# Optimization experiments

Hardware: AMD Instinct MI355X
Metric: run time of the kernel (lower is better)

Reference implementation:

```python
import jax, jax.numpy as jnp
import numpy as np

D_MODEL = 1024
NUM_HEADS = 16
OMEGA_0 = 30.0
D_K = D_MODEL // NUM_HEADS


def _siren_uniform(key, shape, fan_in, omega_0=OMEGA_0):
    bound = np.sqrt(6.0 / fan_in) / omega_0
    return jax.random.uniform(key, shape, minval=-bound, maxval=bound, dtype=jnp.float32)


def setup_inputs() -> dict:
    key = jax.random.key(0)
    ks = jax.random.split(key, 9)
    B, S = 2, 2048
    x = jax.random.normal(ks[0], (B, S, D_MODEL), dtype=jnp.float32)
    # weights stored as (out, in) like torch nn.Linear
    Wq = _siren_uniform(ks[1], (D_MODEL, D_MODEL), D_MODEL)
    bq = _siren_uniform(ks[2], (D_MODEL,), D_MODEL)
    Wk = _siren_uniform(ks[3], (D_MODEL, D_MODEL), D_MODEL)
    bk = _siren_uniform(ks[4], (D_MODEL,), D_MODEL)
    Wv = _siren_uniform(ks[5], (D_MODEL, D_MODEL), D_MODEL)
    bv = _siren_uniform(ks[6], (D_MODEL,), D_MODEL)
    Wo = _siren_uniform(ks[7], (D_MODEL, D_MODEL), D_MODEL)
    bo = _siren_uniform(ks[8], (D_MODEL,), D_MODEL)
    return {"x": x, "Wq": Wq, "bq": bq, "Wk": Wk, "bk": bk,
            "Wv": Wv, "bv": bv, "Wo": Wo, "bo": bo}


def reference(x, Wq, bq, Wk, bk, Wv, bv, Wo, bo):
    B, S, _ = x.shape
    scale = np.sqrt(D_K).astype(np.float32)
    # project and split heads: (B, H, S, d_k)
    def proj(W, b):
        y = jnp.einsum('bsd,ed->bse', x, W) + b
        return y.reshape(B, S, NUM_HEADS, D_K).transpose(0, 2, 1, 3)
    Q = proj(Wq, bq)
    K = proj(Wk, bk)
    V = proj(Wv, bv)
    logits = jnp.einsum('bhqd,bhkd->bhqk', Q, K) / scale
    attn = jnp.sin(OMEGA_0 * logits)  # no normalization
    out = jnp.einsum('bhqk,bhkd->bhqd', attn, V)
    out = out.transpose(0, 2, 1, 3).reshape(B, S, D_MODEL)
    return jnp.einsum('bsd,ed->bse', out, Wo) + bo
```

## Files before the change

### kernel.cpp

```cpp
#include <hip/hip_runtime.h>
#include <stdint.h>

typedef __attribute__((ext_vector_type(8))) __bf16 fragAB;
typedef __attribute__((ext_vector_type(4))) float f32x4;

__device__ __forceinline__ unsigned short f2bf(float f) {
    union { float f; unsigned int u; } v; v.f = f;
    unsigned int u = v.u + 0x7fffu + ((v.u >> 16) & 1u);
    return (unsigned short)(u >> 16);
}

__device__ __forceinline__ f32x4 MFMA(fragAB a, fragAB b, f32x4 c) {
    return __builtin_amdgcn_mfma_f32_16x16x32_bf16(a, b, c, 0, 0, 0);
}

__device__ __forceinline__ void gl16(const void* g, void* l) {
    __builtin_amdgcn_global_load_lds((const __attribute__((address_space(1))) void*)g,
                                     (__attribute__((address_space(3))) void*)l, 16, 0, 0);
}

__device__ __forceinline__ float fsin_rev(float rev) {
    float r; asm("v_sin_f32 %0, %1" : "=v"(r) : "v"(rev)); return r;
}
__device__ __forceinline__ unsigned int cvtpk(float lo, float hi) {
    unsigned int r; asm("v_cvt_pk_bf16_f32 %0, %1, %2" : "=v"(r) : "v"(lo), "v"(hi)); return r;
}

__global__ __launch_bounds__(256) void cvt_all(
    const float* __restrict__ x,  const float* __restrict__ wq, const float* __restrict__ wk,
    const float* __restrict__ wv, const float* __restrict__ wo,
    unsigned short* __restrict__ xb,  unsigned short* __restrict__ wqb, unsigned short* __restrict__ wkb,
    unsigned short* __restrict__ wvb, unsigned short* __restrict__ wob)
{
    const int bid = blockIdx.x;
    const float* s; unsigned short* d; int off;
    if (bid < 4096)      { s = x;  d = xb;  off = bid; }
    else if (bid < 5120) { s = wq; d = wqb; off = bid - 4096; }
    else if (bid < 6144) { s = wk; d = wkb; off = bid - 5120; }
    else if (bid < 7168) { s = wv; d = wvb; off = bid - 6144; }
    else                 { s = wo; d = wob; off = bid - 7168; }
    const int i = (off * 256 + threadIdx.x) * 4;
    float4 f = *(const float4*)(s + i);
    ushort4 o;
    o.x = f2bf(f.x); o.y = f2bf(f.y); o.z = f2bf(f.z); o.w = f2bf(f.w);
    *(ushort4*)(d + i) = o;
}

__global__ __launch_bounds__(256, 2)
void gemm_k(const unsigned short* __restrict__ A,
            const unsigned short* __restrict__ W0, const unsigned short* __restrict__ W1,
            const unsigned short* __restrict__ W2,
            const float* __restrict__ b0, const float* __restrict__ b1, const float* __restrict__ b2,
            void* o0, void* o1, void* o2, int md0, int md1, int md2)
{
    __shared__ unsigned short As[8192];
    __shared__ unsigned short Ws[8192];

    const int z = blockIdx.z;
    const unsigned short* W = z == 0 ? W0 : (z == 1 ? W1 : W2);
    const float* bias        = z == 0 ? b0 : (z == 1 ? b1 : b2);
    void* out                = z == 0 ? o0 : (z == 1 ? o1 : o2);
    const int mode           = z == 0 ? md0 : (z == 1 ? md1 : md2);

    const int t = threadIdx.x;
    const int lane = t & 63;
    const int g = lane >> 4;
    const int c = lane & 15;
    const int w = t >> 6;
    const int wm = (w >> 1) * 64;
    const int wn = (w & 1) * 64;
    const int m0 = blockIdx.y * 128;
    const int n0 = blockIdx.x * 128;

    const int srow = lane >> 3;
    const int scol = (lane & 7) * 8;

    const f32x4 zz = {0.f, 0.f, 0.f, 0.f};
    f32x4 acc[4][4];
#pragma unroll
    for (int mi = 0; mi < 4; ++mi)
#pragma unroll
        for (int ni = 0; ni < 4; ++ni) acc[mi][ni] = zz;

    for (int kt = 0; kt < 16; ++kt) {
        const int k0 = kt * 64;
#pragma unroll
        for (int r = 0; r < 4; ++r) {
            gl16(A + (size_t)(m0 + 32 * w + 8 * r + srow) * 1024 + k0 + scol,
                 (unsigned short*)As + (w * 4 + r) * 512);
            gl16(W + (size_t)(n0 + 32 * w + 8 * r + srow) * 1024 + k0 + scol,
                 (unsigned short*)Ws + (w * 4 + r) * 512);
        }
        __syncthreads();
#pragma unroll
        for (int kk = 0; kk < 2; ++kk) {
            fragAB af[4], bfr[4];
#pragma unroll
            for (int mi = 0; mi < 4; ++mi)
                af[mi] = *(const fragAB*)((char*)As + (wm + mi * 16 + c) * 128 + kk * 64 + g * 16);
#pragma unroll
            for (int ni = 0; ni < 4; ++ni)
                bfr[ni] = *(const fragAB*)((char*)Ws + (wn + ni * 16 + c) * 128 + kk * 64 + g * 16);
#pragma unroll
            for (int mi = 0; mi < 4; ++mi)
#pragma unroll
                for (int ni = 0; ni < 4; ++ni)
                    acc[mi][ni] = MFMA(af[mi], bfr[ni], acc[mi][ni]);
        }
        __syncthreads();
    }

    float bv[4];
#pragma unroll
    for (int ni = 0; ni < 4; ++ni) bv[ni] = bias[n0 + wn + ni * 16 + c];

    if (mode == 0) {
        unsigned short* C = (unsigned short*)out;
#pragma unroll
        for (int mi = 0; mi < 4; ++mi)
#pragma unroll
            for (int ni = 0; ni < 4; ++ni)
#pragma unroll
                for (int j = 0; j < 4; ++j) {
                    const int grow = m0 + wm + mi * 16 + g * 4 + j;
                    const int gcol = n0 + wn + ni * 16 + c;
                    C[(size_t)grow * 1024 + gcol] = f2bf(acc[mi][ni][j] + bv[ni]);
                }
    } else if (mode == 1) {
        unsigned short* Vt = (unsigned short*)out;
#pragma unroll
        for (int mi = 0; mi < 4; ++mi)
#pragma unroll
            for (int ni = 0; ni < 4; ++ni) {
                const int gcol = n0 + wn + ni * 16 + c;
                const int mrow = m0 + wm + mi * 16 + g * 4;
                const int bb = mrow >> 11;
                const int s = mrow & 2047;
                ushort4 pk;
                pk.x = f2bf(acc[mi][ni][0] + bv[ni]);
                pk.y = f2bf(acc[mi][ni][1] + bv[ni]);
                pk.z = f2bf(acc[mi][ni][2] + bv[ni]);
                pk.w = f2bf(acc[mi][ni][3] + bv[ni]);
                *(ushort4*)(Vt + ((size_t)bb * 1024 + gcol) * 2048 + s) = pk;
            }
    } else {
        float* C = (float*)out;
#pragma unroll
        for (int mi = 0; mi < 4; ++mi)
#pragma unroll
            for (int ni = 0; ni < 4; ++ni)
#pragma unroll
                for (int j = 0; j < 4; ++j) {
                    const int grow = m0 + wm + mi * 16 + g * 4 + j;
                    const int gcol = n0 + wn + ni * 16 + c;
                    C[(size_t)grow * 1024 + gcol] = acc[mi][ni][j] + bv[ni];
                }
    }
}

#define SWZ(byteoff, row) ((byteoff) ^ (((row) & 7) << 4))
#define SIN_SC 0.5968310366f

__global__ __launch_bounds__(256, 3)
void attn_kernel(const unsigned short* __restrict__ Qg,
                 const unsigned short* __restrict__ Kg,
                 const unsigned short* __restrict__ Vg,
                 unsigned short* __restrict__ AO)
{
    __shared__ unsigned short Ks[2 * 4096];
    __shared__ unsigned short Vs[2 * 4096];
    __shared__ unsigned short Ps[8192];

    const int t = threadIdx.x;
    const int lane = t & 63;
    const int g = lane >> 4;
    const int c = lane & 15;
    const int w = t >> 6;
    const int qb = blockIdx.x, h = blockIdx.y, b = blockIdx.z;
    const int qbase = qb * 128;

    char* const Ksb = (char*)Ks;
    char* const Vsb = (char*)Vs;
    char* const Psb = (char*)Ps;

    const int rowoff = lane >> 3;
    const int col8 = (lane & 7) ^ rowoff;
    const int ch0 = 2 * w, ch1 = 2 * w + 1;
    const unsigned short* Kg0 = Kg + (size_t)(b * 2048 + 8 * ch0 + rowoff) * 1024 + h * 64 + col8 * 8;
    const unsigned short* Kg1 = Kg + (size_t)(b * 2048 + 8 * ch1 + rowoff) * 1024 + h * 64 + col8 * 8;
    const unsigned short* Vg0 = Vg + ((size_t)b * 1024 + h * 64 + 8 * ch0 + rowoff) * 2048 + col8 * 8;
    const unsigned short* Vg1 = Vg + ((size_t)b * 1024 + h * 64 + 8 * ch1 + rowoff) * 2048 + col8 * 8;

    gl16(Kg0, (unsigned short*)Ks + ch0 * 512);
    gl16(Kg1, (unsigned short*)Ks + ch1 * 512);
    gl16(Vg0, (unsigned short*)Vs + ch0 * 512);
    gl16(Vg1, (unsigned short*)Vs + ch1 * 512);

    fragAB qreg[2][8];
#pragma unroll
    for (int kk = 0; kk < 2; ++kk)
#pragma unroll
        for (int qi = 0; qi < 8; ++qi)
            qreg[kk][qi] = *(const fragAB*)(Qg + (size_t)(b * 2048 + qbase + qi * 16 + c) * 1024
                                            + h * 64 + kk * 32 + g * 8);

    const f32x4 z = {0.f, 0.f, 0.f, 0.f};
    f32x4 o[2][4];
#pragma unroll
    for (int mi = 0; mi < 2; ++mi)
#pragma unroll
        for (int ni = 0; ni < 4; ++ni) o[mi][ni] = z;

    const int krow = 16 * w + c;
    const int pkbyte = (16 * w + g * 4) * 2;

    for (int kb = 0; kb < 32; ++kb) {
        const int cur = kb & 1;
        char* const kc = Ksb + cur * 8192;
        char* const vc = Vsb + cur * 8192;

        __syncthreads();

        if (kb < 31) {
            const int nxt = cur ^ 1;
            unsigned short* kl = (unsigned short*)Ks + nxt * 4096;
            unsigned short* vl = (unsigned short*)Vs + nxt * 4096;
            const size_t ko = (size_t)(kb + 1) * 65536;
            const int vo = (kb + 1) * 64;
            gl16(Kg0 + ko, kl + ch0 * 512);
            gl16(Kg1 + ko, kl + ch1 * 512);
            gl16(Vg0 + vo, vl + ch0 * 512);
            gl16(Vg1 + vo, vl + ch1 * 512);
        }

        fragAB kf0 = *(const fragAB*)(kc + SWZ(krow * 128 + g * 16, krow));
        fragAB kf1 = *(const fragAB*)(kc + SWZ(krow * 128 + 64 + g * 16, krow));
        f32x4 st[8];
#pragma unroll
        for (int qi = 0; qi < 8; ++qi) st[qi] = z;
#pragma unroll
        for (int qi = 0; qi < 8; ++qi) {
            st[qi] = MFMA(kf0, qreg[0][qi], st[qi]);
            st[qi] = MFMA(kf1, qreg[1][qi], st[qi]);
        }

#pragma unroll
        for (int qi = 0; qi < 8; ++qi) {
            const int q = qi * 16 + c;
            float s0 = fsin_rev(st[qi][0] * SIN_SC);
            float s1 = fsin_rev(st[qi][1] * SIN_SC);
            float s2 = fsin_rev(st[qi][2] * SIN_SC);
            float s3 = fsin_rev(st[qi][3] * SIN_SC);
            uint2 pk;
            pk.x = cvtpk(s0, s1);
            pk.y = cvtpk(s2, s3);
            *(uint2*)(Psb + SWZ(q * 128 + pkbyte, q)) = pk;
        }

        asm volatile("s_waitcnt lgkmcnt(0)" ::: "memory");
        __builtin_amdgcn_s_barrier();

#pragma unroll
        for (int kk = 0; kk < 2; ++kk) {
            fragAB pf[2], vf[4];
#pragma unroll
            for (int mi = 0; mi < 2; ++mi) {
                const int q = 32 * w + mi * 16 + c;
                pf[mi] = *(const fragAB*)(Psb + SWZ(q * 128 + kk * 64 + g * 16, q));
            }
#pragma unroll
            for (int ni = 0; ni < 4; ++ni) {
                const int dd = ni * 16 + c;
                vf[ni] = *(const fragAB*)(vc + SWZ(dd * 128 + kk * 64 + g * 16, dd));
            }
#pragma unroll
            for (int mi = 0; mi < 2; ++mi)
#pragma unroll
                for (int ni = 0; ni < 4; ++ni)
                    o[mi][ni] = MFMA(pf[mi], vf[ni], o[mi][ni]);
        }
    }

#pragma unroll
    for (int mi = 0; mi < 2; ++mi)
#pragma unroll
        for (int ni = 0; ni < 4; ++ni) {
            const int dd = ni * 16 + c;
#pragma unroll
            for (int j = 0; j < 4; ++j) {
                const int q = qbase + 32 * w + mi * 16 + g * 4 + j;
                AO[(size_t)(b * 2048 + q) * 1024 + h * 64 + dd] = f2bf(o[mi][ni][j]);
            }
        }
}

extern "C" void kernel_launch(void* const* d_in, const int* in_sizes, int n_in,
                              void* d_out, int out_size, void* d_ws, size_t ws_size,
                              hipStream_t stream) {
    (void)in_sizes; (void)n_in; (void)out_size; (void)ws_size;
    const float* x  = (const float*)d_in[0];
    const float* Wq = (const float*)d_in[1];
    const float* bq = (const float*)d_in[2];
    const float* Wk = (const float*)d_in[3];
    const float* bk = (const float*)d_in[4];
    const float* Wv = (const float*)d_in[5];
    const float* bv = (const float*)d_in[6];
    const float* Wo = (const float*)d_in[7];
    const float* bo = (const float*)d_in[8];

    char* ws = (char*)d_ws;
    unsigned short* xb  = (unsigned short*)(ws);
    unsigned short* Wqb = (unsigned short*)(ws + (8u  << 20));
    unsigned short* Wkb = (unsigned short*)(ws + (10u << 20));
    unsigned short* Wvb = (unsigned short*)(ws + (12u << 20));
    unsigned short* Wob = (unsigned short*)(ws + (14u << 20));
    unsigned short* Qb  = (unsigned short*)(ws + (16u << 20));
    unsigned short* Kb  = (unsigned short*)(ws + (24u << 20));
    unsigned short* Vtb = (unsigned short*)(ws + (32u << 20));
    unsigned short* AO  = (unsigned short*)(ws + (40u << 20));

    cvt_all<<<8192, 256, 0, stream>>>(x, Wq, Wk, Wv, Wo, xb, Wqb, Wkb, Wvb, Wob);

    gemm_k<<<dim3(8, 32, 3), 256, 0, stream>>>(xb, Wqb, Wkb, Wvb, bq, bk, bv,
                                               Qb, Kb, Vtb, 0, 0, 1);

    attn_kernel<<<dim3(16, 16, 2), 256, 0, stream>>>(Qb, Kb, Vtb, AO);

    gemm_k<<<dim3(8, 32, 1), 256, 0, stream>>>(AO, Wob, Wob, Wob, bo, bo, bo,
                                               d_out, d_out, d_out, 2, 2, 2);
}
```

Baseline: 125.0 us.

## Software-pipeline attention loop with triple-buffered K/V and double-buffered P

Restructures the attention main loop into a software pipeline: each iteration computes S=QK^T and sin for block kb while doing the P·V product for block kb-1. K and V move to triple-buffered LDS and P to double-buffered LDS, and global prefetch runs two K blocks and one V block ahead, synchronised with vmcnt waits and a single barrier per iteration. The aim is to overlap the sin/transcendental work with the PV MFMAs and to drop one barrier per iteration. The cost is more LDS (about 80KB), which lowers the occupancy target from 3 to 2 blocks per CU, plus extra prologue and epilogue code and more complex buffer index bookkeeping.

```diff
diff --git a/kernel.cpp b/kernel.cpp
--- a/kernel.cpp
+++ b/kernel.cpp
@@ -161,15 +161,15 @@
 #define SWZ(byteoff, row) ((byteoff) ^ (((row) & 7) << 4))
 #define SIN_SC 0.5968310366f
 
-__global__ __launch_bounds__(256, 3)
+__global__ __launch_bounds__(256, 2)
 void attn_kernel(const unsigned short* __restrict__ Qg,
                  const unsigned short* __restrict__ Kg,
                  const unsigned short* __restrict__ Vg,
                  unsigned short* __restrict__ AO)
 {
-    __shared__ unsigned short Ks[2 * 4096];
-    __shared__ unsigned short Vs[2 * 4096];
-    __shared__ unsigned short Ps[8192];
+    __shared__ unsigned short Ks[3 * 4096];
+    __shared__ unsigned short Vs[3 * 4096];
+    __shared__ unsigned short Ps[2 * 8192];
 
     const int t = threadIdx.x;
     const int lane = t & 63;
@@ -191,11 +191,6 @@
     const unsigned short* Vg0 = Vg + ((size_t)b * 1024 + h * 64 + 8 * ch0 + rowoff) * 2048 + col8 * 8;
     const unsigned short* Vg1 = Vg + ((size_t)b * 1024 + h * 64 + 8 * ch1 + rowoff) * 2048 + col8 * 8;
 
-    gl16(Kg0, (unsigned short*)Ks + ch0 * 512);
-    gl16(Kg1, (unsigned short*)Ks + ch1 * 512);
-    gl16(Vg0, (unsigned short*)Vs + ch0 * 512);
-    gl16(Vg1, (unsigned short*)Vs + ch1 * 512);
-
     fragAB qreg[2][8];
 #pragma unroll
     for (int kk = 0; kk < 2; ++kk)
@@ -203,6 +198,17 @@
         for (int qi = 0; qi < 8; ++qi)
             qreg[kk][qi] = *(const fragAB*)(Qg + (size_t)(b * 2048 + qbase + qi * 16 + c) * 1024
                                             + h * 64 + kk * 32 + g * 8);
+    asm volatile("s_waitcnt vmcnt(0)" ::: "memory");
+
+    {
+        gl16(Kg0, (unsigned short*)Ks + ch0 * 512);
+        gl16(Kg1, (unsigned short*)Ks + ch1 * 512);
+        gl16(Vg0, (unsigned short*)Vs + ch0 * 512);
+        gl16(Vg1, (unsigned short*)Vs + ch1 * 512);
+        gl16(Kg0 + 65536, (unsigned short*)Ks + 4096 + ch0 * 512);
+        gl16(Kg1 + 65536, (unsigned short*)Ks + 4096 + ch1 * 512);
+    }
+    asm volatile("s_waitcnt vmcnt(4)" ::: "memory");
 
     const f32x4 z = {0.f, 0.f, 0.f, 0.f};
     f32x4 o[2][4];
@@ -214,25 +220,24 @@
     const int krow = 16 * w + c;
     const int pkbyte = (16 * w + g * 4) * 2;
 
+    int bK = 0;
     for (int kb = 0; kb < 32; ++kb) {
-        const int cur = kb & 1;
-        char* const kc = Ksb + cur * 8192;
-        char* const vc = Vsb + cur * 8192;
-
-        __syncthreads();
-
-        if (kb < 31) {
-            const int nxt = cur ^ 1;
-            unsigned short* kl = (unsigned short*)Ks + nxt * 4096;
-            unsigned short* vl = (unsigned short*)Vs + nxt * 4096;
-            const size_t ko = (size_t)(kb + 1) * 65536;
-            const int vo = (kb + 1) * 64;
-            gl16(Kg0 + ko, kl + ch0 * 512);
-            gl16(Kg1 + ko, kl + ch1 * 512);
-            gl16(Vg0 + vo, vl + ch0 * 512);
-            gl16(Vg1 + vo, vl + ch1 * 512);
-        }
-
+        const int bKw = bK == 0 ? 2 : bK - 1;
+        const int bVw = bK == 2 ? 0 : bK + 1;
+        const int bVr = bKw;
+
+        {
+            const int vn = (kb + 1) & 31;
+            const int kn = (kb + 2) & 31;
+            unsigned short* vl = (unsigned short*)Vs + bVw * 4096;
+            unsigned short* kl = (unsigned short*)Ks + bKw * 4096;
+            gl16(Vg0 + vn * 64, vl + ch0 * 512);
+            gl16(Vg1 + vn * 64, vl + ch1 * 512);
+            gl16(Kg0 + (size_t)kn * 65536, kl + ch0 * 512);
+            gl16(Kg1 + (size_t)kn * 65536, kl + ch1 * 512);
+        }
+
+        char* const kc = Ksb + bK * 8192;
         fragAB kf0 = *(const fragAB*)(kc + SWZ(krow * 128 + g * 16, krow));
         fragAB kf1 = *(const fragAB*)(kc + SWZ(krow * 128 + 64 + g * 16, krow));
         f32x4 st[8];
@@ -244,6 +249,7 @@
             st[qi] = MFMA(kf1, qreg[1][qi], st[qi]);
         }
 
+        char* const pw = Psb + (kb & 1) * 16384;
 #pragma unroll
         for (int qi = 0; qi < 8; ++qi) {
             const int q = qi * 16 + c;
@@ -254,19 +260,50 @@
             uint2 pk;
             pk.x = cvtpk(s0, s1);
             pk.y = cvtpk(s2, s3);
-            *(uint2*)(Psb + SWZ(q * 128 + pkbyte, q)) = pk;
+            *(uint2*)(pw + SWZ(q * 128 + pkbyte, q)) = pk;
+        }
+
+        if (kb > 0) {
+            char* const pr = Psb + ((kb - 1) & 1) * 16384;
+            char* const vc = Vsb + bVr * 8192;
+#pragma unroll
+            for (int kk = 0; kk < 2; ++kk) {
+                fragAB pf[2], vf[4];
+#pragma unroll
+                for (int mi = 0; mi < 2; ++mi) {
+                    const int q = 32 * w + mi * 16 + c;
+                    pf[mi] = *(const fragAB*)(pr + SWZ(q * 128 + kk * 64 + g * 16, q));
+                }
+#pragma unroll
+                for (int ni = 0; ni < 4; ++ni) {
+                    const int dd = ni * 16 + c;
+                    vf[ni] = *(const fragAB*)(vc + SWZ(dd * 128 + kk * 64 + g * 16, dd));
+                }
+#pragma unroll
+                for (int mi = 0; mi < 2; ++mi)
+#pragma unroll
+                    for (int ni = 0; ni < 4; ++ni)
+                        o[mi][ni] = MFMA(pf[mi], vf[ni], o[mi][ni]);
+            }
         }
 
         asm volatile("s_waitcnt lgkmcnt(0)" ::: "memory");
+        asm volatile("s_waitcnt vmcnt(4)" ::: "memory");
         __builtin_amdgcn_s_barrier();
 
+        bK = bK == 2 ? 0 : bK + 1;
+    }
+
+    {
+        char* const pr = Psb + 16384;
+        char* const vc = Vsb + 8192;
 #pragma unroll
         for (int kk = 0; kk < 2; ++kk) {
             fragAB pf[2], vf[4];
 #pragma unroll
             for (int mi = 0; mi < 2; ++mi) {
                 const int q = 32 * w + mi * 16 + c;
-                pf[mi] = *(const fragAB*)(Psb + SWZ(q * 128 + kk * 64 + g * 16, q));
+                pf[mi] = *(const fragAB*)(pr + SWZ(q * 128 + kk * 64 + g * 16, q));
             }
 #pragma unroll
             for (int ni = 0; ni < 4; ++ni) {
```

Measured after the change: 125.6 us. No clear change (+0.5%).

## Halve attention query tile, remap blocks for head locality, add 64-row output GEMM

Applied to the files above, without the earlier changes.

The attention kernel now processes 64 query rows per block instead of 128, doubling the grid to 1024 blocks. It uses a 1D grid with a swizzled block-to-(b,h,q) mapping, so blocks sharing K/V tiles run together, and a smaller P buffer to allow higher occupancy. A dedicated gemm64 kernel with 64x128 tiles replaces the generic GEMM for the output projection, giving more blocks for better CU fill. The trade-off is that each attention block now reloads K/V for half as many queries, roughly doubling K/V traffic, and barrier placement moves to the end of each iteration.

```diff
diff --git a/kernel.cpp b/kernel.cpp
--- a/kernel.cpp
+++ b/kernel.cpp
@@ -51,7 +51,7 @@
             const unsigned short* __restrict__ W0, const unsigned short* __restrict__ W1,
             const unsigned short* __restrict__ W2,
             const float* __restrict__ b0, const float* __restrict__ b1, const float* __restrict__ b2,
-            void* o0, void* o1, void* o2, int md0, int md1, int md2)
+            void* o0, void* o1, void* o2)
 {
     __shared__ unsigned short As[8192];
     __shared__ unsigned short Ws[8192];
@@ -60,7 +60,7 @@
     const unsigned short* W = z == 0 ? W0 : (z == 1 ? W1 : W2);
     const float* bias        = z == 0 ? b0 : (z == 1 ? b1 : b2);
     void* out                = z == 0 ? o0 : (z == 1 ? o1 : o2);
-    const int mode           = z == 0 ? md0 : (z == 1 ? md1 : md2);
+    const int mode           = z == 2 ? 1 : 0;
 
     const int t = threadIdx.x;
     const int lane = t & 63;
@@ -126,7 +126,7 @@
                     const int gcol = n0 + wn + ni * 16 + c;
                     C[(size_t)grow * 1024 + gcol] = f2bf(acc[mi][ni][j] + bv[ni]);
                 }
-    } else if (mode == 1) {
+    } else {
         unsigned short* Vt = (unsigned short*)out;
 #pragma unroll
         for (int mi = 0; mi < 4; ++mi)
@@ -143,25 +143,84 @@
                 pk.w = f2bf(acc[mi][ni][3] + bv[ni]);
                 *(ushort4*)(Vt + ((size_t)bb * 1024 + gcol) * 2048 + s) = pk;
             }
-    } else {
-        float* C = (float*)out;
-#pragma unroll
-        for (int mi = 0; mi < 4; ++mi)
+    }
+}
+
+__global__ __launch_bounds__(256, 4)
+void gemm64(const unsigned short* __restrict__ A,
+            const unsigned short* __restrict__ W,
+            const float* __restrict__ bias, float* __restrict__ out)
+{
+    __shared__ unsigned short As[4096];
+    __shared__ unsigned short Ws[8192];
+
+    const int t = threadIdx.x;
+    const int lane = t & 63;
+    const int g = lane >> 4;
+    const int c = lane & 15;
+    const int w = t >> 6;
+    const int wm = (w >> 1) * 32;
+    const int wn = (w & 1) * 64;
+    const int m0 = blockIdx.y * 64;
+    const int n0 = blockIdx.x * 128;
+
+    const int srow = lane >> 3;
+    const int scol = (lane & 7) * 8;
+
+    const f32x4 zz = {0.f, 0.f, 0.f, 0.f};
+    f32x4 acc[2][4];
+#pragma unroll
+    for (int mi = 0; mi < 2; ++mi)
+#pragma unroll
+        for (int ni = 0; ni < 4; ++ni) acc[mi][ni] = zz;
+
+    for (int kt = 0; kt < 16; ++kt) {
+        const int k0 = kt * 64;
+        gl16(A + (size_t)(m0 + 16 * w + srow) * 1024 + k0 + scol,
+             (unsigned short*)As + (2 * w) * 512);
+        gl16(A + (size_t)(m0 + 16 * w + 8 + srow) * 1024 + k0 + scol,
+             (unsigned short*)As + (2 * w + 1) * 512);
+#pragma unroll
+        for (int r = 0; r < 4; ++r)
+            gl16(W + (size_t)(n0 + 32 * w + 8 * r + srow) * 1024 + k0 + scol,
+                 (unsigned short*)Ws + (w * 4 + r) * 512);
+        __syncthreads();
+#pragma unroll
+        for (int kk = 0; kk < 2; ++kk) {
+            fragAB af[2], bfr[4];
+#pragma unroll
+            for (int mi = 0; mi < 2; ++mi)
+                af[mi] = *(const fragAB*)((char*)As + (wm + mi * 16 + c) * 128 + kk * 64 + g * 16);
 #pragma unroll
             for (int ni = 0; ni < 4; ++ni)
-#pragma unroll
-                for (int j = 0; j < 4; ++j) {
-                    const int grow = m0 + wm + mi * 16 + g * 4 + j;
-                    const int gcol = n0 + wn + ni * 16 + c;
-                    C[(size_t)grow * 1024 + gcol] = acc[mi][ni][j] + bv[ni];
-                }
+                bfr[ni] = *(const fragAB*)((char*)Ws + (wn + ni * 16 + c) * 128 + kk * 64 + g * 16);
+#pragma unroll
+            for (int mi = 0; mi < 2; ++mi)
+#pragma unroll
+                for (int ni = 0; ni < 4; ++ni)
+                    acc[mi][ni] = MFMA(af[mi], bfr[ni], acc[mi][ni]);
+        }
+        __syncthreads();
+    }
+
+#pragma unroll
+    for (int ni = 0; ni < 4; ++ni) {
+        const float bv = bias[n0 + wn + ni * 16 + c];
+#pragma unroll
+        for (int mi = 0; mi < 2; ++mi)
+#pragma unroll
+            for (int j = 0; j < 4; ++j) {
+                const int grow = m0 + wm + mi * 16 + g * 4 + j;
+                const int gcol = n0 + wn + ni * 16 + c;
+                out[(size_t)grow * 1024 + gcol] = acc[mi][ni][j] + bv;
+            }
     }
 }
 
 #define SWZ(byteoff, row) ((byteoff) ^ (((row) & 7) << 4))
 #define SIN_SC 0.5968310366f
 
-__global__ __launch_bounds__(256, 3)
+__global__ __launch_bounds__(256, 4)
 void attn_kernel(const unsigned short* __restrict__ Qg,
                  const unsigned short* __restrict__ Kg,
                  const unsigned short* __restrict__ Vg,
@@ -169,47 +228,49 @@
 {
     __shared__ unsigned short Ks[2 * 4096];
     __shared__ unsigned short Vs[2 * 4096];
-    __shared__ unsigned short Ps[8192];
+    __shared__ unsigned short Ps[4096];
 
     const int t = threadIdx.x;
     const int lane = t & 63;
     const int g = lane >> 4;
     const int c = lane & 15;
     const int w = t >> 6;
-    const int qb = blockIdx.x, h = blockIdx.y, b = blockIdx.z;
-    const int qbase = qb * 128;
+
+    const int bid = blockIdx.x;
+    const int lb = (bid & 7) * 128 + (bid >> 3);
+    const int qb = lb & 31;
+    const int h = (lb >> 5) & 15;
+    const int b = lb >> 9;
+    const int qbase = qb * 64;
 
     char* const Ksb = (char*)Ks;
     char* const Vsb = (char*)Vs;
     char* const Psb = (char*)Ps;
 
-    const int rowoff = lane >> 3;
-    const int col8 = (lane & 7) ^ rowoff;
+    const int r8 = lane >> 3;
+    const int col8 = (lane & 7) ^ r8;
+    const unsigned short* KgB = Kg + (size_t)(b * 2048) * 1024 + h * 64;
+    const unsigned short* VtB = Vg + ((size_t)b * 1024 + h * 64) * 2048;
     const int ch0 = 2 * w, ch1 = 2 * w + 1;
-    const unsigned short* Kg0 = Kg + (size_t)(b * 2048 + 8 * ch0 + rowoff) * 1024 + h * 64 + col8 * 8;
-    const unsigned short* Kg1 = Kg + (size_t)(b * 2048 + 8 * ch1 + rowoff) * 1024 + h * 64 + col8 * 8;
-    const unsigned short* Vg0 = Vg + ((size_t)b * 1024 + h * 64 + 8 * ch0 + rowoff) * 2048 + col8 * 8;
-    const unsigned short* Vg1 = Vg + ((size_t)b * 1024 + h * 64 + 8 * ch1 + rowoff) * 2048 + col8 * 8;
-
-    gl16(Kg0, (unsigned short*)Ks + ch0 * 512);
-    gl16(Kg1, (unsigned short*)Ks + ch1 * 512);
-    gl16(Vg0, (unsigned short*)Vs + ch0 * 512);
-    gl16(Vg1, (unsigned short*)Vs + ch1 * 512);
-
-    fragAB qreg[2][8];
+
+    fragAB qreg[2][4];
 #pragma unroll
     for (int kk = 0; kk < 2; ++kk)
 #pragma unroll
-        for (int qi = 0; qi < 8; ++qi)
+        for (int qi = 0; qi < 4; ++qi)
             qreg[kk][qi] = *(const fragAB*)(Qg + (size_t)(b * 2048 + qbase + qi * 16 + c) * 1024
                                             + h * 64 + kk * 32 + g * 8);
 
+    gl16(KgB + (size_t)(8 * ch0 + r8) * 1024 + col8 * 8, (unsigned short*)Ks + ch0 * 512);
+    gl16(KgB + (size_t)(8 * ch1 + r8) * 1024 + col8 * 8, (unsigned short*)Ks + ch1 * 512);
+    gl16(VtB + (size_t)(8 * ch0 + r8) * 2048 + col8 * 8, (unsigned short*)Vs + ch0 * 512);
+    gl16(VtB + (size_t)(8 * ch1 + r8) * 2048 + col8 * 8, (unsigned short*)Vs + ch1 * 512);
+    __syncthreads();
+
     const f32x4 z = {0.f, 0.f, 0.f, 0.f};
-    f32x4 o[2][4];
-#pragma unroll
-    for (int mi = 0; mi < 2; ++mi)
-#pragma unroll
-        for (int ni = 0; ni < 4; ++ni) o[mi][ni] = z;
+    f32x4 o[4];
+#pragma unroll
+    for (int ni = 0; ni < 4; ++ni) o[ni] = z;
 
     const int krow = 16 * w + c;
     const int pkbyte = (16 * w + g * 4) * 2;
@@ -219,33 +280,30 @@
         char* const kc = Ksb + cur * 8192;
         char* const vc = Vsb + cur * 8192;
 
-        __syncthreads();
-
         if (kb < 31) {
             const int nxt = cur ^ 1;
             unsigned short* kl = (unsigned short*)Ks + nxt * 4096;
             unsigned short* vl = (unsigned short*)Vs + nxt * 4096;
-            const size_t ko = (size_t)(kb + 1) * 65536;
-            const int vo = (kb + 1) * 64;
-            gl16(Kg0 + ko, kl + ch0 * 512);
-            gl16(Kg1 + ko, kl + ch1 * 512);
-            gl16(Vg0 + vo, vl + ch0 * 512);
-            gl16(Vg1 + vo, vl + ch1 * 512);
+            const size_t kro = (size_t)(kb + 1) * 64;
+            gl16(KgB + (kro + 8 * ch0 + r8) * 1024 + col8 * 8, kl + ch0 * 512);
+            gl16(KgB + (kro + 8 * ch1 + r8) * 1024 + col8 * 8, kl + ch1 * 512);
+            gl16(VtB + (size_t)(8 * ch0 + r8) * 2048 + kro + col8 * 8, vl + ch0 * 512);
+            gl16(VtB + (size_t)(8 * ch1 + r8) * 2048 + kro + col8 * 8, vl + ch1 * 512);
         }
 
         fragAB kf0 = *(const fragAB*)(kc + SWZ(krow * 128 + g * 16, krow));
         fragAB kf1 = *(const fragAB*)(kc + SWZ(krow * 128 + 64 + g * 16, krow));
-        f32x4 st[8];
-#pragma unroll
-        for (int qi = 0; qi < 8; ++qi) st[qi] = z;
-#pragma unroll
-        for (int qi = 0; qi < 8; ++qi) {
+        f32x4 st[4];
+#pragma unroll
+        for (int qi = 0; qi < 4; ++qi) st[qi] = z;
+#pragma unroll
+        for (int qi = 0; qi < 4; ++qi) {
             st[qi] = MFMA(kf0, qreg[0][qi], st[qi]);
             st[qi] = MFMA(kf1, qreg[1][qi], st[qi]);
         }
 
 #pragma unroll
-        for (int qi = 0; qi < 8; ++qi) {
+        for (int qi = 0; qi < 4; ++qi) {
             const int q = qi * 16 + c;
             float s0 = fsin_rev(st[qi][0] * SIN_SC);
             float s1 = fsin_rev(st[qi][1] * SIN_SC);
@@ -262,36 +320,30 @@
 
 #pragma unroll
         for (int kk = 0; kk < 2; ++kk) {
-            fragAB pf[2], vf[4];
-#pragma unroll
-            for (int mi = 0; mi < 2; ++mi) {
-                const int q = 32 * w + mi * 16 + c;
-                pf[mi] = *(const fragAB*)(Psb + SWZ(q * 128 + kk * 64 + g * 16, q));
-            }
+            fragAB pf, vf[4];
+            pf = *(const fragAB*)(Psb + SWZ(krow * 128 + kk * 64 + g * 16, krow));
 #pragma unroll
             for (int ni = 0; ni < 4; ++ni) {
                 const int dd = ni * 16 + c;
                 vf[ni] = *(const fragAB*)(vc + SWZ(dd * 128 + kk * 64 + g * 16, dd));
             }
 #pragma unroll
-            for (int mi = 0; mi < 2; ++mi)
-#pragma unroll
-                for (int ni = 0; ni < 4; ++ni)
-                    o[mi][ni] = MFMA(pf[mi], vf[ni], o[mi][ni]);
-        }
-    }
-
-#pragma unroll
-    for (int mi = 0; mi < 2; ++mi)
-#pragma unroll
-        for (int ni = 0; ni < 4; ++ni) {
-            const int dd = ni * 16 + c;
-#pragma unroll
-            for (int j = 0; j < 4; ++j) {
-                const int q = qbase + 32 * w + mi * 16 + g * 4 + j;
-                AO[(size_t)(b * 2048 + q) * 1024 + h * 64 + dd] = f2bf(o[mi][ni][j]);
-            }
-        }
+            for (int ni = 0; ni < 4; ++ni)
+                o[ni] = MFMA(pf, vf[ni], o[ni]);
+        }
+
+        __syncthreads();
+    }
+
+#pragma unroll
+    for (int ni = 0; ni < 4; ++ni) {
+        const int dd = ni * 16 + c;
+#pragma unroll
+        for (int j = 0; j < 4; ++j) {
+            const int q = qbase + 16 * w + g * 4 + j;
+            AO[(size_t)(b * 2048 + q) * 1024 + h * 64 + dd] = f2bf(o[ni][j]);
+        }
+    }
 }
 
 extern "C" void kernel_launch(void* const* d_in, const int* in_sizes, int n_in,
@@ -322,10 +374,9 @@
     cvt_all<<<8192, 256, 0, stream>>>(x, Wq, Wk, Wv, Wo, xb, Wqb, Wkb, Wvb, Wob);
 
     gemm_k<<<dim3(8, 32, 3), 256, 0, stream>>>(xb, Wqb, Wkb, Wvb, bq, bk, bv,
-                                               Qb, Kb, Vtb, 0, 0, 1);
-
-    attn_kernel<<<dim3(16, 16, 2), 256, 0, stream>>>(Qb, Kb, Vtb, AO);
-
-    gemm_k<<<dim3(8, 32, 1), 256, 0, stream>>>(AO, Wob, Wob, Wob, bo, bo, bo,
-                                               d_out, d_out, d_out, 2, 2, 2);
-}
+                                               Qb, Kb, Vtb);
+
+    attn_kernel<<<1024, 256, 0, stream>>>(Qb, Kb, Vtb, AO);
+
+    gemm64<<<dim3(8, 64), 256, 0, stream>>>(AO, Wob, bo, (float*)d_out);
+}
```

Result: faster. 116.3 us (-7.0%).
